# Kernel tuning notes

Hardware: AMD Instinct MI355X
Metric: run time of the kernel (lower is better)

Reference implementation:

```python
import jax, jax.numpy as jnp
import numpy as np

NUM_HEADS = 16
ROPE_THETA = 10000.0


def _rope_cos_sin(seq_len, head_dim, dtype):
    # theta_i = theta^(-2i/d_k), i in [0, d_k/2)
    i = jnp.arange(head_dim // 2, dtype=jnp.float32)
    inv_freq = ROPE_THETA ** (-2.0 * i / head_dim)
    pos = jnp.arange(seq_len, dtype=jnp.float32)[:, None]
    ang = pos * inv_freq[None, :]                      # [S, d/2]
    return jnp.cos(ang).astype(dtype), jnp.sin(ang).astype(dtype)


def _apply_rope(t, cos, sin):
    # t: [B, H, S, d]; rotate consecutive pairs (complex multiply)
    B, H, S, d = t.shape
    tp = t.reshape(B, H, S, d // 2, 2)
    x0, x1 = tp[..., 0], tp[..., 1]
    r0 = x0 * cos - x1 * sin
    r1 = x0 * sin + x1 * cos
    return jnp.stack([r0, r1], axis=-1).reshape(B, H, S, d)


def setup_inputs() -> dict:
    key = jax.random.key(0)
    k1, k2, k3 = jax.random.split(key, 3)
    B, S, D = 4, 2048, 1024
    x = jax.random.normal(k1, (B, S, D), dtype=jnp.float32)
    padding_mask = jnp.ones((B, S), dtype=jnp.int32)
    # trunc-normal-ish init, std = sqrt(2/(in+out))
    std_qkv = np.sqrt(2.0 / (D + 3 * D))
    w_qkv = jax.random.normal(k2, (3 * D, D), dtype=jnp.float32) * std_qkv
    w_o = jax.random.normal(k3, (D, D), dtype=jnp.float32) * 0.02
    return {"x": x, "padding_mask": padding_mask, "w_qkv": w_qkv, "w_o": w_o}


def reference(x, padding_mask, w_qkv, w_o):
    B, S, D = x.shape
    H = NUM_HEADS
    hd = D // H
    scale = 1.0 / np.sqrt(hd)

    qkv = x @ w_qkv.T                                   # [B, S, 3D]
    q, k, v = jnp.split(qkv, 3, axis=-1)

    def to_heads(t):
        return t.reshape(B, S, H, hd).transpose(0, 2, 1, 3)  # [B, H, S, hd]

    q, k, v = to_heads(q), to_heads(k), to_heads(v)

    cos, sin = _rope_cos_sin(S, hd, x.dtype)            # [S, hd/2]
    q = _apply_rope(q, cos, sin)
    k = _apply_rope(k, cos, sin)

    scores = jnp.einsum("bhqd,bhkd->bhqk", q, k) * scale  # [B, H, S, S]

    causal = jnp.tril(jnp.ones((S, S), dtype=x.dtype))
    mask = causal[None, :, :] * padding_mask.astype(x.dtype)[:, None, :]  # [B, S, S]
    scores = jnp.where(mask[:, None, :, :] == 0, -jnp.inf, scores)

    weights = jax.nn.softmax(scores, axis=-1)
    out = jnp.einsum("bhqk,bhkd->bhqd", weights, v)     # [B, H, S, hd]
    out = out.transpose(0, 2, 1, 3).reshape(B, S, D)
    return out @ w_o.T
```

## Files before the change

kernel.cpp:

```cpp
#include <hip/hip_runtime.h>

typedef unsigned short u16;
typedef unsigned int u32;
typedef __bf16 bf16x8 __attribute__((ext_vector_type(8)));
typedef float f32x4 __attribute__((ext_vector_type(4)));
typedef float f32x16 __attribute__((ext_vector_type(16)));
typedef u32 u32x4 __attribute__((ext_vector_type(4)));

#define MFMA_BF16(a, b, c) __builtin_amdgcn_mfma_f32_16x16x32_bf16((a), (b), (c), 0, 0, 0)
#define MFMA32(a, b, c) __builtin_amdgcn_mfma_f32_32x32x16_bf16((a), (b), (c), 0, 0, 0)

#define QSCALE 0.18033688011112042f

#define BARRIER __builtin_amdgcn_s_barrier()
#define LGKM0                                                \
  do {                                                       \
    asm volatile("s_waitcnt lgkmcnt(0)" ::: "memory");       \
    __builtin_amdgcn_sched_barrier(0);                       \
  } while (0)
#define WAIT_VM(N) asm volatile("s_waitcnt vmcnt(" #N ")" ::: "memory")


__device__ __forceinline__ u16 f2bf(float f) {
  u32 u = __builtin_bit_cast(u32, f);
  u += 0x7fffu + ((u >> 16) & 1u);
  return (u16)(u >> 16);
}

__device__ __forceinline__ void async_copy16(const void* g, void* l) {
  __builtin_amdgcn_global_load_lds(
      (__attribute__((address_space(1))) void*)g,
      (__attribute__((address_space(3))) void*)l, 16, 0, 0);
}

__device__ __forceinline__ u32 cvt_pk_bf16(float lo, float hi) {
  u32 d;
  asm("v_cvt_pk_bf16_f32 %0, %1, %2" : "=v"(d) : "v"(lo), "v"(hi));
  return d;
}

__device__ __forceinline__ void swap32(u32& a, u32& b) {
  asm("v_permlane32_swap_b32 %0, %1" : "+v"(a), "+v"(b));
}


__global__ __launch_bounds__(256) void prep_kernel(
    const float* __restrict__ x_f, const float* __restrict__ wqkv_f,
    const float* __restrict__ wo_f, u16* __restrict__ xb,
    u16* __restrict__ wqkvb, u16* __restrict__ wob, float2* __restrict__ rope_t) {
  const int blk = blockIdx.x;
  if (blk < 12288) {
    const float* src;
    u16* dst;
    int base;
    float scale = 1.0f;
    if (blk < 8192)      { src = x_f;    dst = xb;    base = blk; }
    else if (blk < 11264){ src = wqkv_f; dst = wqkvb; base = blk - 8192;
                           if (base < 1024) scale = QSCALE; }
    else                 { src = wo_f;   dst = wob;   base = blk - 11264; }
    const int i = base * 1024 + threadIdx.x * 4;
    const float4 v = *(const float4*)(src + i);
    ushort4 o;
    o.x = f2bf(v.x * scale); o.y = f2bf(v.y * scale);
    o.z = f2bf(v.z * scale); o.w = f2bf(v.w * scale);
    *(ushort4*)(dst + i) = o;
  } else {
    const int idx = (blk - 12288) * 256 + threadIdx.x;
    const int s = idx >> 5, i = idx & 31;
    const float invf = __builtin_amdgcn_exp2f(-(float)i * 0.41524101186092027f);
    float rev = (float)s * invf * 0.15915494309189535f;
    rev -= floorf(rev);
    rope_t[idx] = make_float2(__builtin_amdgcn_cosf(rev), __builtin_amdgcn_sinf(rev));
  }
}


__device__ __forceinline__ void gemm256_bt(const u16* __restrict__ A,
                                           const u16* __restrict__ B,
                                           int row0, int col0, u16* lds,
                                           f32x4 acc[4][4]) {
  const int tid = threadIdx.x;
  const int wave = tid >> 6, lane = tid & 63;
  const int fr = lane & 15, quad = lane >> 4;
  const int wm = (wave >> 1) * 64;
  const int wn = (wave & 1) * 64;
  u16* bufA0 = lds;
  u16* bufB0 = lds + 16384;
  u16* bufA1 = lds + 24576;
  u16* bufB1 = lds + 40960;

  const int l8 = lane >> 3, l7 = lane & 7;
  const int csw = (l7 ^ l8) * 8;

  f32x4 zero = {0.f, 0.f, 0.f, 0.f};
#pragma unroll
  for (int mt = 0; mt < 4; ++mt)
#pragma unroll
    for (int nt = 0; nt < 4; ++nt) acc[mt][nt] = zero;

  auto stage = [&](int t) {
    u16* ba = (t & 1) ? bufA1 : bufA0;
    u16* bb = (t & 1) ? bufB1 : bufB0;
    const int k0 = t * 64;
#pragma unroll
    for (int c = 0; c < 4; ++c) {
      const int ch = c * 8 + wave;
      async_copy16(A + (size_t)(row0 + ch * 8 + l8) * 1024 + k0 + csw,
                   ba + ch * 512);
    }
#pragma unroll
    for (int c = 0; c < 2; ++c) {
      const int ch = c * 8 + wave;
      async_copy16(B + (size_t)(col0 + ch * 8 + l8) * 1024 + k0 + csw,
                   bb + ch * 512);
    }
  };

  const int f7 = fr & 7;
  const int sw0 = (quad ^ f7) * 8;
  const int sw1 = ((quad + 4) ^ f7) * 8;
  const int ar0 = (wm + fr) * 64, ar1 = (wm + 16 + fr) * 64;
  const int ar2 = (wm + 32 + fr) * 64, ar3 = (wm + 48 + fr) * 64;
  const int br0 = (wn + fr) * 64, br1 = (wn + 16 + fr) * 64;
  const int br2 = (wn + 32 + fr) * 64, br3 = (wn + 48 + fr) * 64;

  stage(0);
  stage(1);
  WAIT_VM(6);
  BARRIER;

  for (int t = 0; t < 16; ++t) {
    const u16* ba = (t & 1) ? bufA1 : bufA0;
    const u16* bb = (t & 1) ? bufB1 : bufB0;

    bf16x8 a0k0 = *(const bf16x8*)(ba + ar0 + sw0);
    bf16x8 a0k1 = *(const bf16x8*)(ba + ar0 + sw1);
    bf16x8 a1k0 = *(const bf16x8*)(ba + ar1 + sw0);
    bf16x8 a1k1 = *(const bf16x8*)(ba + ar1 + sw1);
    bf16x8 b0k0 = *(const bf16x8*)(bb + br0 + sw0);
    bf16x8 b0k1 = *(const bf16x8*)(bb + br0 + sw1);
    bf16x8 b1k0 = *(const bf16x8*)(bb + br1 + sw0);
    bf16x8 b1k1 = *(const bf16x8*)(bb + br1 + sw1);
    BARRIER;
    LGKM0;
    __builtin_amdgcn_s_setprio(1);
    acc[0][0] = MFMA_BF16(a0k0, b0k0, acc[0][0]);
    acc[0][1] = MFMA_BF16(a0k0, b1k0, acc[0][1]);
    acc[1][0] = MFMA_BF16(a1k0, b0k0, acc[1][0]);
    acc[1][1] = MFMA_BF16(a1k0, b1k0, acc[1][1]);
    acc[0][0] = MFMA_BF16(a0k1, b0k1, acc[0][0]);
    acc[0][1] = MFMA_BF16(a0k1, b1k1, acc[0][1]);
    acc[1][0] = MFMA_BF16(a1k1, b0k1, acc[1][0]);
    acc[1][1] = MFMA_BF16(a1k1, b1k1, acc[1][1]);
    __builtin_amdgcn_s_setprio(0);
    BARRIER;

    bf16x8 b2k0 = *(const bf16x8*)(bb + br2 + sw0);
    bf16x8 b2k1 = *(const bf16x8*)(bb + br2 + sw1);
    bf16x8 b3k0 = *(const bf16x8*)(bb + br3 + sw0);
    bf16x8 b3k1 = *(const bf16x8*)(bb + br3 + sw1);
    BARRIER;
    LGKM0;
    __builtin_amdgcn_s_setprio(1);
    acc[0][2] = MFMA_BF16(a0k0, b2k0, acc[0][2]);
    acc[0][3] = MFMA_BF16(a0k0, b3k0, acc[0][3]);
    acc[1][2] = MFMA_BF16(a1k0, b2k0, acc[1][2]);
    acc[1][3] = MFMA_BF16(a1k0, b3k0, acc[1][3]);
    acc[0][2] = MFMA_BF16(a0k1, b2k1, acc[0][2]);
    acc[0][3] = MFMA_BF16(a0k1, b3k1, acc[0][3]);
    acc[1][2] = MFMA_BF16(a1k1, b2k1, acc[1][2]);
    acc[1][3] = MFMA_BF16(a1k1, b3k1, acc[1][3]);
    __builtin_amdgcn_s_setprio(0);
    BARRIER;

    bf16x8 a2k0 = *(const bf16x8*)(ba + ar2 + sw0);
    bf16x8 a2k1 = *(const bf16x8*)(ba + ar2 + sw1);
    bf16x8 a3k0 = *(const bf16x8*)(ba + ar3 + sw0);
    bf16x8 a3k1 = *(const bf16x8*)(ba + ar3 + sw1);
    BARRIER;
    LGKM0;
    __builtin_amdgcn_s_setprio(1);
    acc[2][0] = MFMA_BF16(a2k0, b0k0, acc[2][0]);
    acc[2][1] = MFMA_BF16(a2k0, b1k0, acc[2][1]);
    acc[3][0] = MFMA_BF16(a3k0, b0k0, acc[3][0]);
    acc[3][1] = MFMA_BF16(a3k0, b1k0, acc[3][1]);
    acc[2][0] = MFMA_BF16(a2k1, b0k1, acc[2][0]);
    acc[2][1] = MFMA_BF16(a2k1, b1k1, acc[2][1]);
    acc[3][0] = MFMA_BF16(a3k1, b0k1, acc[3][0]);
    acc[3][1] = MFMA_BF16(a3k1, b1k1, acc[3][1]);
    acc[2][2] = MFMA_BF16(a2k0, b2k0, acc[2][2]);
    acc[2][3] = MFMA_BF16(a2k0, b3k0, acc[2][3]);
    acc[3][2] = MFMA_BF16(a3k0, b2k0, acc[3][2]);
    acc[3][3] = MFMA_BF16(a3k0, b3k0, acc[3][3]);
    acc[2][2] = MFMA_BF16(a2k1, b2k1, acc[2][2]);
    acc[2][3] = MFMA_BF16(a2k1, b3k1, acc[2][3]);
    acc[3][2] = MFMA_BF16(a3k1, b2k1, acc[3][2]);
    acc[3][3] = MFMA_BF16(a3k1, b3k1, acc[3][3]);
    __builtin_amdgcn_s_setprio(0);

    BARRIER;
    if (t + 2 < 16) {
      stage(t + 2);
      WAIT_VM(6);
    } else if (t + 2 == 16) {
      WAIT_VM(0);
    }
    BARRIER;
  }
}


__global__ __launch_bounds__(512, 2) void qkv_rope_kernel(
    const u16* __restrict__ x, const u16* __restrict__ w_qkv,
    const float2* __restrict__ rope_t,
    u16* __restrict__ q_ws, u16* __restrict__ k_ws, u16* __restrict__ vt_ws) {
  __shared__ u16 lds[49152];
  f32x4 acc[4][4];
  const int lin0 = blockIdx.x + 24 * blockIdx.y;
  const int lin = (lin0 & 7) * 96 + (lin0 >> 3);
  const int row0 = (lin / 24) * 256;
  const int col0 = (lin % 24) * 128;
  gemm256_bt(x, w_qkv, row0, col0, lds, acc);

  const int tid = threadIdx.x;
  const int wave = tid >> 6, lane = tid & 63;
  const int fr = lane & 15, quad = lane >> 4;
  const int wm = (wave >> 1) * 64, wn = (wave & 1) * 64;
  const int region = col0 >> 10;
  const int f0 = col0 & 1023;
  const int s0r = row0 & 2047;
  const int bb = row0 >> 11;
  const int h0 = f0 >> 6;

  if (region < 2) {
#pragma unroll
    for (int mt = 0; mt < 4; ++mt) {
#pragma unroll
      for (int nt = 0; nt < 4; ++nt) {
        const int n = wn + nt * 16 + fr;
        const int d = n & 63;
#pragma unroll
        for (int r = 0; r < 4; ++r) {
          const int m = wm + mt * 16 + quad * 4 + r;
          const float own = acc[mt][nt][r];
          const float part = __shfl_xor(own, 1);
          const int s = s0r + m;
          const float2 cssn = rope_t[s * 32 + (d >> 1)];
          const float val = (d & 1) ? (part * cssn.y + own * cssn.x)
                                    : (own * cssn.x - part * cssn.y);
          lds[m * 136 + n] = f2bf(val);
        }
      }
    }
    __syncthreads();
    u16* dst = (region == 0) ? q_ws : k_ws;
#pragma unroll
    for (int j = 0; j < 8; ++j) {
      const int idx2 = j * 512 + tid;
      const int m = idx2 >> 4;
      const int rem = idx2 & 15;
      const int hf = rem >> 3;
      const int c8 = (rem & 7) * 8;
      const uint4 v = *(const uint4*)(lds + m * 136 + hf * 64 + c8);
      *(uint4*)(dst + ((size_t)(bb * 16 + h0 + hf) * 2048 + s0r + m) * 64 + c8) = v;
    }
  } else {
#pragma unroll
    for (int mt = 0; mt < 4; ++mt)
#pragma unroll
      for (int nt = 0; nt < 4; ++nt) {
        const int n = wn + nt * 16 + fr;
#pragma unroll
        for (int r = 0; r < 4; ++r) {
          const int m = wm + mt * 16 + quad * 4 + r;
          lds[n * 264 + m] = f2bf(acc[mt][nt][r]);
        }
      }
    __syncthreads();
#pragma unroll
    for (int j = 0; j < 8; ++j) {
      const int idx2 = j * 512 + tid;
      const int n = idx2 >> 5;
      const int mc = (idx2 & 31) * 8;
      const int h = h0 + (n >> 6);
      const int d = n & 63;
      const uint4 v = *(const uint4*)(lds + n * 264 + mc);
      *(uint4*)(vt_ws + ((size_t)(bb * 16 + h) * 64 + d) * 2048 + s0r + mc) = v;
    }
  }
}


__global__ __launch_bounds__(256, 3) void flash_attn_kernel(
    const u16* __restrict__ Q, const u16* __restrict__ K, const u16* __restrict__ Vt,
    const int* __restrict__ pad, u16* __restrict__ O) {
  const int S = 2048;
  const int idx = blockIdx.x;
  const int bh = idx & 63;
  const int b = bh >> 4, h = bh & 15;
  const int j = (idx >> 6) & 3;
  const int sr = idx >> 8;
  const int qt_rev = (sr >> 1) * 8 + ((sr & 1) ? (7 - j) : j);
  const int q0 = (15 - qt_rev) * 128;
  const u16* Qh = Q + (size_t)bh * S * 64;
  const u16* Kh = K + (size_t)bh * S * 64;
  const u16* Vth = Vt + (size_t)bh * 64 * S;
  const int tid = threadIdx.x, wave = tid >> 6, lane = tid & 63;
  const int l31 = lane & 31, hi = lane >> 5, l7 = lane & 7;

  __shared__ u16 lds_k[2][64 * 64];
  __shared__ u16 lds_vt[2][64 * 64];
  __shared__ float lds_biasf[2][64];

  const int qb = q0 + wave * 32;

  bf16x8 qfrag[4];
#pragma unroll
  for (int c = 0; c < 4; ++c)
    qfrag[c] = *(const bf16x8*)(Qh + (size_t)(qb + l31) * 64 + c * 16 + hi * 8);

  bf16x8 ones;
#pragma unroll
  for (int jj = 0; jj < 8; ++jj) ones[jj] = (__bf16)1.0f;

  f32x16 o_acc0, o_acc1, lacc;
#pragma unroll
  for (int r = 0; r < 16; ++r) { o_acc0[r] = 0.f; o_acc1[r] = 0.f; lacc[r] = 0.f; }

  const float NEG = -__builtin_inff();
  int pv0 = 1, pv1 = 1;

  auto stage = [&](int k0, int bufi) {
#pragma unroll
    for (int it = 0; it < 2; ++it) {
      const int slot = it * 256 + tid;
      const int row = slot >> 3;
      const int g = slot & 7;
      const int gs = (g ^ (row & 7)) * 8;
      async_copy16(Kh + (size_t)(k0 + row) * 64 + gs, &lds_k[bufi][slot * 8]);
      async_copy16(Vth + (size_t)row * 2048 + k0 + gs, &lds_vt[bufi][slot * 8]);
    }
    if (tid < 64) lds_biasf[bufi][tid] = pad[b * S + k0 + tid] ? 0.f : NEG;
    const int pvn = pad[b * S + k0 + lane];
    if (bufi) pv1 = pvn; else pv0 = pvn;
  };

  const int kend = q0 + 64;
  stage(0, 0);
  __syncthreads();
  int cur = 0;

  for (int k0 = 0; k0 <= kend; k0 += 64) {
    if (k0 < kend) stage(k0 + 64, cur ^ 1);

    if (k0 <= qb + 31) {
      const u16* lk = lds_k[cur];
      const u16* lvt = lds_vt[cur];
      const float* lb = lds_biasf[cur];
      const int pvc = cur ? pv1 : pv0;
      const bool fast = (__ballot(pvc != 0) == ~0ull);
      const bool needMask = (k0 + 63 > qb);
      const int thrh = qb + l31 - k0 - 4 * hi;

      f32x16 sacc0, sacc1;
#pragma unroll
      for (int r = 0; r < 16; ++r) { sacc0[r] = 0.f; sacc1[r] = 0.f; }
#pragma unroll
      for (int c = 0; c < 4; ++c) {
        const int gsw = ((2 * c + hi) ^ l7) * 8;
        bf16x8 kf0 = *(const bf16x8*)(lk + l31 * 64 + gsw);
        bf16x8 kf1 = *(const bf16x8*)(lk + (l31 + 32) * 64 + gsw);
        sacc0 = MFMA32(kf0, qfrag[c], sacc0);
        sacc1 = MFMA32(kf1, qfrag[c], sacc1);
      }

      bf16x8 pa[2][2];
#pragma unroll
      for (int kt = 0; kt < 2; ++kt) {
        float pe[16];
        if (fast) {
#pragma unroll
          for (int r = 0; r < 16; ++r) {
            float s = (kt == 0) ? sacc0[r] : sacc1[r];
            if (needMask) {
              const int rm = (r & 3) + 8 * (r >> 2) + 32 * kt;
              s = (rm > thrh) ? NEG : s;
            }
            pe[r] = __builtin_amdgcn_exp2f(s);
          }
        } else {
          f32x4 bv[4];
#pragma unroll
          for (int g = 0; g < 4; ++g)
            bv[g] = *(const f32x4*)(lb + g * 8 + 4 * hi + 32 * kt);
#pragma unroll
          for (int r = 0; r < 16; ++r) {
            float s = ((kt == 0) ? sacc0[r] : sacc1[r]) + bv[r >> 2][r & 3];
            if (needMask) {
              const int rm = (r & 3) + 8 * (r >> 2) + 32 * kt;
              s = (rm > thrh) ? NEG : s;
            }
            pe[r] = __builtin_amdgcn_exp2f(s);
          }
        }
        u32 a0 = cvt_pk_bf16(pe[0], pe[1]), a1 = cvt_pk_bf16(pe[2], pe[3]);
        u32 b0 = cvt_pk_bf16(pe[4], pe[5]), b1 = cvt_pk_bf16(pe[6], pe[7]);
        swap32(a0, b0);
        swap32(a1, b1);
        u32x4 w0 = {a0, a1, b0, b1};
        pa[kt][0] = __builtin_bit_cast(bf16x8, w0);
        u32 c0 = cvt_pk_bf16(pe[8], pe[9]), c1 = cvt_pk_bf16(pe[10], pe[11]);
        u32 d0 = cvt_pk_bf16(pe[12], pe[13]), d1 = cvt_pk_bf16(pe[14], pe[15]);
        swap32(c0, d0);
        swap32(c1, d1);
        u32x4 w1 = {c0, c1, d0, d1};
        pa[kt][1] = __builtin_bit_cast(bf16x8, w1);
      }

      __builtin_amdgcn_s_setprio(1);
#pragma unroll
      for (int kt = 0; kt < 2; ++kt)
#pragma unroll
        for (int ks = 0; ks < 2; ++ks) {
          const int kq = kt * 2 + ks;
          lacc = MFMA32(pa[kt][ks], ones, lacc);
          const int gsw = ((2 * kq + hi) ^ l7) * 8;
          bf16x8 vf0 = *(const bf16x8*)(lvt + l31 * 64 + gsw);
          bf16x8 vf1 = *(const bf16x8*)(lvt + (l31 + 32) * 64 + gsw);
          o_acc0 = MFMA32(pa[kt][ks], vf0, o_acc0);
          o_acc1 = MFMA32(pa[kt][ks], vf1, o_acc1);
        }
      __builtin_amdgcn_s_setprio(0);
    }

    __syncthreads();
    cur ^= 1;
  }

#pragma unroll
  for (int r = 0; r < 16; ++r) {
    const int q = qb + (r & 3) + 8 * (r >> 2) + 4 * hi;
    const float l = lacc[r];
    const float rl = (l > 0.f) ? (1.0f / l) : 0.f;
    O[(size_t)(b * S + q) * 1024 + h * 64 + l31] = f2bf(o_acc0[r] * rl);
    O[(size_t)(b * S + q) * 1024 + h * 64 + 32 + l31] = f2bf(o_acc1[r] * rl);
  }
}


__global__ __launch_bounds__(512, 2) void oproj_kernel(
    const u16* __restrict__ A, const u16* __restrict__ w_o, float* __restrict__ out) {
  __shared__ u16 lds[49152];
  f32x4 acc[4][4];
  const int row0 = blockIdx.y * 256;
  const int col0 = blockIdx.x * 128;
  gemm256_bt(A, w_o, row0, col0, lds, acc);
  const int tid = threadIdx.x;
  const int wave = tid >> 6, lane = tid & 63;
  const int fr = lane & 15, quad = lane >> 4;
  const int wm = (wave >> 1) * 64, wn = (wave & 1) * 64;
#pragma unroll
  for (int mt = 0; mt < 4; ++mt)
#pragma unroll
    for (int nt = 0; nt < 4; ++nt) {
      const int ncol = col0 + wn + nt * 16 + fr;
#pragma unroll
      for (int r = 0; r < 4; ++r) {
        const int mrow = row0 + wm + mt * 16 + quad * 4 + r;
        out[(size_t)mrow * 1024 + ncol] = acc[mt][nt][r];
      }
    }
}


extern "C" void kernel_launch(void* const* d_in, const int* in_sizes, int n_in,
                              void* d_out, int out_size, void* d_ws, size_t ws_size,
                              hipStream_t stream) {
  const float* x_f = (const float*)d_in[0];
  const int* pad = (const int*)d_in[1];
  const float* wqkv_f = (const float*)d_in[2];
  const float* wo_f = (const float*)d_in[3];
  float* out = (float*)d_out;

  const int NX = 4 * 2048 * 1024;
  const int NWQKV = 3072 * 1024;
  const int NWO = 1024 * 1024;
  const size_t HSZ = (size_t)4 * 16 * 2048 * 64;

  u16* xb = (u16*)d_ws;
  u16* wqkvb = xb + NX;
  u16* wob = wqkvb + NWQKV;
  u16* q_ws = wob + NWO;
  u16* k_ws = q_ws + HSZ;
  u16* vt_ws = k_ws + HSZ;
  u16* attn_ws = vt_ws + HSZ;
  float2* rope_t = (float2*)(attn_ws + HSZ);

  prep_kernel<<<dim3(12544), dim3(256), 0, stream>>>(x_f, wqkv_f, wo_f, xb, wqkvb,
                                                     wob, rope_t);
  qkv_rope_kernel<<<dim3(24, 32), dim3(512), 0, stream>>>(xb, wqkvb, rope_t, q_ws,
                                                          k_ws, vt_ws);
  flash_attn_kernel<<<dim3(1024), dim3(256), 0, stream>>>(q_ws, k_ws, vt_ws, pad,
                                                          attn_ws);
  oproj_kernel<<<dim3(8, 32), dim3(512), 0, stream>>>(attn_ws, wob, out);
}
```

Measured before the change: 253.2 us.

## Rewrite projection GEMM mainloop as triple-buffered K=32 pipeline with higher occupancy

The shared 256x128 GEMM helper changes from a double-buffered K=64 loop with many barriers and XOR-swizzled LDS to a triple-buffered K=32 loop. Each iteration loads all A/B fragments, issues the next prefetch, runs 16 MFMAs, and uses a single barrier. LDS per block drops to 72KB and launch bounds allow 4 blocks per CU, both meant to hide latency better. The swizzle is removed, so the unswizzled 64-byte row layout may cause LDS bank conflicts, and the register cap for 4 waves per SIMD may cause spills.

```diff
diff --git a/kernel.cpp b/kernel.cpp
--- a/kernel.cpp
+++ b/kernel.cpp
@@ -75,22 +75,15 @@
 }
 
 
-__device__ __forceinline__ void gemm256_bt(const u16* __restrict__ A,
-                                           const u16* __restrict__ B,
-                                           int row0, int col0, u16* lds,
-                                           f32x4 acc[4][4]) {
+__device__ __forceinline__ void gemm_tb(const u16* __restrict__ A,
+                                        const u16* __restrict__ B,
+                                        int row0, int col0, u16* lds,
+                                        f32x4 acc[4][4]) {
   const int tid = threadIdx.x;
   const int wave = tid >> 6, lane = tid & 63;
   const int fr = lane & 15, quad = lane >> 4;
   const int wm = (wave >> 1) * 64;
   const int wn = (wave & 1) * 64;
-  u16* bufA0 = lds;
-  u16* bufB0 = lds + 16384;
-  u16* bufA1 = lds + 24576;
-  u16* bufB1 = lds + 40960;
-
-  const int l8 = lane >> 3, l7 = lane & 7;
-  const int csw = (l7 ^ l8) * 8;
 
   f32x4 zero = {0.f, 0.f, 0.f, 0.f};
 #pragma unroll
@@ -99,128 +92,64 @@
     for (int nt = 0; nt < 4; ++nt) acc[mt][nt] = zero;
 
   auto stage = [&](int t) {
-    u16* ba = (t & 1) ? bufA1 : bufA0;
-    u16* bb = (t & 1) ? bufB1 : bufB0;
-    const int k0 = t * 64;
-#pragma unroll
-    for (int c = 0; c < 4; ++c) {
-      const int ch = c * 8 + wave;
-      async_copy16(A + (size_t)(row0 + ch * 8 + l8) * 1024 + k0 + csw,
-                   ba + ch * 512);
-    }
-#pragma unroll
-    for (int c = 0; c < 2; ++c) {
-      const int ch = c * 8 + wave;
-      async_copy16(B + (size_t)(col0 + ch * 8 + l8) * 1024 + k0 + csw,
-                   bb + ch * 512);
-    }
+    u16* base = lds + (t % 3) * 12288;
+    const int k0 = t * 32;
+#pragma unroll
+    for (int it = 0; it < 2; ++it) {
+      const int slot = it * 512 + tid;
+      const int row = slot >> 2, g = slot & 3;
+      async_copy16(A + (size_t)(row0 + row) * 1024 + k0 + g * 8, base + slot * 8);
+    }
+    const int row = tid >> 2, g = tid & 3;
+    async_copy16(B + (size_t)(col0 + row) * 1024 + k0 + g * 8,
+                 base + 8192 + tid * 8);
   };
 
-  const int f7 = fr & 7;
-  const int sw0 = (quad ^ f7) * 8;
-  const int sw1 = ((quad + 4) ^ f7) * 8;
-  const int ar0 = (wm + fr) * 64, ar1 = (wm + 16 + fr) * 64;
-  const int ar2 = (wm + 32 + fr) * 64, ar3 = (wm + 48 + fr) * 64;
-  const int br0 = (wn + fr) * 64, br1 = (wn + 16 + fr) * 64;
-  const int br2 = (wn + 32 + fr) * 64, br3 = (wn + 48 + fr) * 64;
-
+  const int aoff = fr * 32 + quad * 8;
   stage(0);
   stage(1);
-  WAIT_VM(6);
+  WAIT_VM(3);
   BARRIER;
 
-  for (int t = 0; t < 16; ++t) {
-    const u16* ba = (t & 1) ? bufA1 : bufA0;
-    const u16* bb = (t & 1) ? bufB1 : bufB0;
-
-    bf16x8 a0k0 = *(const bf16x8*)(ba + ar0 + sw0);
-    bf16x8 a0k1 = *(const bf16x8*)(ba + ar0 + sw1);
-    bf16x8 a1k0 = *(const bf16x8*)(ba + ar1 + sw0);
-    bf16x8 a1k1 = *(const bf16x8*)(ba + ar1 + sw1);
-    bf16x8 b0k0 = *(const bf16x8*)(bb + br0 + sw0);
-    bf16x8 b0k1 = *(const bf16x8*)(bb + br0 + sw1);
-    bf16x8 b1k0 = *(const bf16x8*)(bb + br1 + sw0);
-    bf16x8 b1k1 = *(const bf16x8*)(bb + br1 + sw1);
-    BARRIER;
+  for (int t = 0; t < 32; ++t) {
+    const u16* bs = lds + (t % 3) * 12288;
+
+    bf16x8 a[4], b[4];
+#pragma unroll
+    for (int m = 0; m < 4; ++m)
+      a[m] = *(const bf16x8*)(bs + (wm + m * 16) * 32 + aoff);
+#pragma unroll
+    for (int n = 0; n < 4; ++n)
+      b[n] = *(const bf16x8*)(bs + 8192 + (wn + n * 16) * 32 + aoff);
+
+    if (t + 2 < 32) stage(t + 2);
+
     LGKM0;
     __builtin_amdgcn_s_setprio(1);
-    acc[0][0] = MFMA_BF16(a0k0, b0k0, acc[0][0]);
-    acc[0][1] = MFMA_BF16(a0k0, b1k0, acc[0][1]);
-    acc[1][0] = MFMA_BF16(a1k0, b0k0, acc[1][0]);
-    acc[1][1] = MFMA_BF16(a1k0, b1k0, acc[1][1]);
-    acc[0][0] = MFMA_BF16(a0k1, b0k1, acc[0][0]);
-    acc[0][1] = MFMA_BF16(a0k1, b1k1, acc[0][1]);
-    acc[1][0] = MFMA_BF16(a1k1, b0k1, acc[1][0]);
-    acc[1][1] = MFMA_BF16(a1k1, b1k1, acc[1][1]);
+#pragma unroll
+    for (int m = 0; m < 4; ++m)
+#pragma unroll
+      for (int n = 0; n < 4; ++n)
+        acc[m][n] = MFMA_BF16(a[m], b[n], acc[m][n]);
     __builtin_amdgcn_s_setprio(0);
-    BARRIER;
-
-    bf16x8 b2k0 = *(const bf16x8*)(bb + br2 + sw0);
-    bf16x8 b2k1 = *(const bf16x8*)(bb + br2 + sw1);
-    bf16x8 b3k0 = *(const bf16x8*)(bb + br3 + sw0);
-    bf16x8 b3k1 = *(const bf16x8*)(bb + br3 + sw1);
-    BARRIER;
-    LGKM0;
-    __builtin_amdgcn_s_setprio(1);
-    acc[0][2] = MFMA_BF16(a0k0, b2k0, acc[0][2]);
-    acc[0][3] = MFMA_BF16(a0k0, b3k0, acc[0][3]);
-    acc[1][2] = MFMA_BF16(a1k0, b2k0, acc[1][2]);
-    acc[1][3] = MFMA_BF16(a1k0, b3k0, acc[1][3]);
-    acc[0][2] = MFMA_BF16(a0k1, b2k1, acc[0][2]);
-    acc[0][3] = MFMA_BF16(a0k1, b3k1, acc[0][3]);
-    acc[1][2] = MFMA_BF16(a1k1, b2k1, acc[1][2]);
-    acc[1][3] = MFMA_BF16(a1k1, b3k1, acc[1][3]);
-    __builtin_amdgcn_s_setprio(0);
-    BARRIER;
-
-    bf16x8 a2k0 = *(const bf16x8*)(ba + ar2 + sw0);
-    bf16x8 a2k1 = *(const bf16x8*)(ba + ar2 + sw1);
-    bf16x8 a3k0 = *(const bf16x8*)(ba + ar3 + sw0);
-    bf16x8 a3k1 = *(const bf16x8*)(ba + ar3 + sw1);
-    BARRIER;
-    LGKM0;
-    __builtin_amdgcn_s_setprio(1);
-    acc[2][0] = MFMA_BF16(a2k0, b0k0, acc[2][0]);
-    acc[2][1] = MFMA_BF16(a2k0, b1k0, acc[2][1]);
-    acc[3][0] = MFMA_BF16(a3k0, b0k0, acc[3][0]);
-    acc[3][1] = MFMA_BF16(a3k0, b1k0, acc[3][1]);
-    acc[2][0] = MFMA_BF16(a2k1, b0k1, acc[2][0]);
-    acc[2][1] = MFMA_BF16(a2k1, b1k1, acc[2][1]);
-    acc[3][0] = MFMA_BF16(a3k1, b0k1, acc[3][0]);
-    acc[3][1] = MFMA_BF16(a3k1, b1k1, acc[3][1]);
-    acc[2][2] = MFMA_BF16(a2k0, b2k0, acc[2][2]);
-    acc[2][3] = MFMA_BF16(a2k0, b3k0, acc[2][3]);
-    acc[3][2] = MFMA_BF16(a3k0, b2k0, acc[3][2]);
-    acc[3][3] = MFMA_BF16(a3k0, b3k0, acc[3][3]);
-    acc[2][2] = MFMA_BF16(a2k1, b2k1, acc[2][2]);
-    acc[2][3] = MFMA_BF16(a2k1, b3k1, acc[2][3]);
-    acc[3][2] = MFMA_BF16(a3k1, b2k1, acc[3][2]);
-    acc[3][3] = MFMA_BF16(a3k1, b3k1, acc[3][3]);
-    __builtin_amdgcn_s_setprio(0);
-
-    BARRIER;
-    if (t + 2 < 16) {
-      stage(t + 2);
-      WAIT_VM(6);
-    } else if (t + 2 == 16) {
-      WAIT_VM(0);
-    }
+
+    if (t + 2 < 32) { WAIT_VM(3); } else { WAIT_VM(0); }
     BARRIER;
   }
 }
 
 
-__global__ __launch_bounds__(512, 2) void qkv_rope_kernel(
+__global__ __launch_bounds__(512, 4) void qkv_rope_kernel(
     const u16* __restrict__ x, const u16* __restrict__ w_qkv,
     const float2* __restrict__ rope_t,
     u16* __restrict__ q_ws, u16* __restrict__ k_ws, u16* __restrict__ vt_ws) {
-  __shared__ u16 lds[49152];
+  __shared__ u16 lds[36864];
   f32x4 acc[4][4];
   const int lin0 = blockIdx.x + 24 * blockIdx.y;
   const int lin = (lin0 & 7) * 96 + (lin0 >> 3);
   const int row0 = (lin / 24) * 256;
   const int col0 = (lin % 24) * 128;
-  gemm256_bt(x, w_qkv, row0, col0, lds, acc);
+  gemm_tb(x, w_qkv, row0, col0, lds, acc);
 
   const int tid = threadIdx.x;
   const int wave = tid >> 6, lane = tid & 63;
@@ -448,13 +377,13 @@
 }
 
 
-__global__ __launch_bounds__(512, 2) void oproj_kernel(
+__global__ __launch_bounds__(512, 4) void oproj_kernel(
     const u16* __restrict__ A, const u16* __restrict__ w_o, float* __restrict__ out) {
-  __shared__ u16 lds[49152];
+  __shared__ u16 lds[36864];
   f32x4 acc[4][4];
   const int row0 = blockIdx.y * 256;
   const int col0 = blockIdx.x * 128;
-  gemm256_bt(A, w_o, row0, col0, lds, acc);
+  gemm_tb(A, w_o, row0, col0, lds, acc);
   const int tid = threadIdx.x;
   const int wave = tid >> 6, lane = tid & 63;
   const int fr = lane & 15, quad = lane >> 4;
```

New measurement: 243.9 us. 3.7% less time.
